# Kernel optimization log

Hardware: AMD Instinct MI355X
Metric: run time of the kernel (lower is better)

Reference implementation:

```python
import jax, jax.numpy as jnp
import numpy as np

IN_CHANNELS = 8
CHANNELS = 8
MASK_OUT_STRIDE = 4


def aligned_bilinear(x, factor):
    # Faithful port of AdelaiDet aligned_bilinear (align_corners=True).
    if factor == 1:
        return x
    n, c, h, w = x.shape
    x = jnp.pad(x, ((0, 0), (0, 0), (0, 1), (0, 1)), mode='edge')
    oh, ow = factor * h + 1, factor * w + 1

    def interp_axis(arr, out_len, axis):
        # align_corners=True from size s+1 -> factor*s+1: src coord = i / factor
        coords = jnp.arange(out_len) / factor
        i0 = jnp.floor(coords).astype(jnp.int32)
        i1 = jnp.minimum(i0 + 1, arr.shape[axis] - 1)
        t = (coords - i0).astype(arr.dtype)
        a0 = jnp.take(arr, i0, axis=axis)
        a1 = jnp.take(arr, i1, axis=axis)
        shp = [1] * arr.ndim
        shp[axis] = out_len
        t = t.reshape(shp)
        return a0 * (1 - t) + a1 * t

    x = interp_axis(x, oh, 2)
    x = interp_axis(x, ow, 3)
    p = factor // 2
    x = jnp.pad(x, ((0, 0), (0, 0), (p, 0), (p, 0)), mode='edge')
    return x[:, :, : oh - 1, : ow - 1]


def setup_inputs() -> dict:
    key = jax.random.key(0)
    ks = jax.random.split(key, 6)
    N, C, H, W = 4, IN_CHANNELS, 112, 200
    n_inst = 200
    stride = 8
    num_gen_params = (C + 2) * CHANNELS + CHANNELS + CHANNELS * CHANNELS + CHANNELS + CHANNELS + 1  # 169
    mask_feats = jax.random.normal(ks[0], (N, C, H, W), dtype=jnp.float32)
    mask_head_params = jax.random.normal(ks[1], (n_inst, num_gen_params), dtype=jnp.float32) * 0.1
    # instance centers anywhere inside the image (in input-image pixel coords)
    instance_locations = jax.random.uniform(ks[2], (n_inst, 2), dtype=jnp.float32) * jnp.array(
        [W * stride, H * stride], dtype=jnp.float32)
    sizes_of_interest = jnp.array([64.0, 128.0, 256.0, 512.0, 1024.0], dtype=jnp.float32)
    im_inds = jax.random.randint(ks[3], (n_inst,), 0, N, dtype=jnp.int32)
    fpn_levels = jax.random.randint(ks[4], (n_inst,), 0, 5, dtype=jnp.int32)
    return {
        'mask_feats': mask_feats,
        'mask_head_params': mask_head_params,
        'instance_locations': instance_locations,
        'sizes_of_interest': sizes_of_interest,
        'im_inds': im_inds,
        'fpn_levels': fpn_levels,
        'mask_feat_stride': stride,
    }


def reference(mask_feats, mask_head_params, instance_locations, sizes_of_interest,
              im_inds, fpn_levels, mask_feat_stride):
    N, C, H, W = mask_feats.shape
    n_inst = mask_head_params.shape[0]
    HW = H * W
    stride = mask_feat_stride  # python int

    # compute_locations: (x, y) pairs, x fastest, at pixel centers (stride//2 offset)
    xs = (jnp.arange(W) * stride + stride // 2).astype(mask_feats.dtype)
    ys = (jnp.arange(H) * stride + stride // 2).astype(mask_feats.dtype)
    gx, gy = jnp.meshgrid(xs, ys, indexing='xy')  # [H, W]
    locations = jnp.stack([gx, gy], axis=-1).reshape(HW, 2)  # [HW, 2]

    # relative coords, normalized by size-of-interest per instance
    rel = instance_locations[:, None, :] - locations[None, :, :]  # [n, HW, 2]
    rel = jnp.transpose(rel, (0, 2, 1))  # [n, 2, HW]
    soi = sizes_of_interest[fpn_levels]  # [n]
    rel = rel / soi[:, None, None]

    feats = mask_feats[im_inds].reshape(n_inst, C, HW)  # [n, C, HW]
    x = jnp.concatenate([rel, feats], axis=1)  # [n, C+2, HW]

    # parse_dynamic_params: split [n, 169] into per-layer 1x1 conv weights/biases
    wn = [(C + 2) * CHANNELS, CHANNELS * CHANNELS, CHANNELS * 1]
    bn = [CHANNELS, CHANNELS, 1]
    sizes = wn + bn
    offs = np.cumsum([0] + sizes)
    parts = [mask_head_params[:, offs[i]:offs[i + 1]] for i in range(len(sizes))]
    w0 = parts[0].reshape(n_inst, CHANNELS, C + 2)
    w1 = parts[1].reshape(n_inst, CHANNELS, CHANNELS)
    w2 = parts[2].reshape(n_inst, 1, CHANNELS)
    b0, b1, b2 = parts[3], parts[4], parts[5]

    # per-instance grouped 1x1 convs == batched matmuls over instances
    x = jax.nn.relu(jnp.einsum('noi,nip->nop', w0, x) + b0[:, :, None])
    x = jax.nn.relu(jnp.einsum('noi,nip->nop', w1, x) + b1[:, :, None])
    x = jnp.einsum('noi,nip->nop', w2, x) + b2[:, :, None]  # [n, 1, HW]

    mask_logits = x.reshape(n_inst, 1, H, W)
    factor = stride // MASK_OUT_STRIDE
    return aligned_bilinear(mask_logits, factor)
```

## Files before the change

### kernel.cpp

```cpp
#include <hip/hip_runtime.h>


#define IN_C   8
#define CHN    8
#define Hh     112
#define Ww     200
#define HWp    (Hh * Ww)
#define OH     224
#define OW     400
#define TY     16
#define RL     9
#define NPIX   (RL * Ww)
#define NPAIR  (NPIX / 2)
#define NTILES (OH / TY)
#define NPARAMS 169

typedef __fp16 f16x2 __attribute__((ext_vector_type(2)));


__global__ __launch_bounds__(256, 4)
void dmh_fused_kernel(const float* __restrict__ feats,
                      const float* __restrict__ params,
                      const float* __restrict__ iloc,
                      const float* __restrict__ soi_tab,
                      const int*   __restrict__ im_inds,
                      const int*   __restrict__ fpn_levels,
                      float* __restrict__ out)
{
    __shared__ uint  h0s[CHN][NPAIR];
    __shared__ float lgt[RL][Ww];

    const int bid  = blockIdx.x;
    const int inst = bid / NTILES;
    const int ty   = bid - inst * NTILES;
    const int y0   = ty * TY;
    const int r_lo = (y0 > 0 ? (y0 - 1) : 0) >> 1;
    const int tid  = threadIdx.x;

    const float* __restrict__ wp = params + inst * NPARAMS;
    const float soi    = soi_tab[fpn_levels[inst]];
    const float inv_s  = 1.0f / soi;
    const float ix     = iloc[inst * 2 + 0];
    const float iy     = iloc[inst * 2 + 1];
    const float* __restrict__ fb = feats + (size_t)im_inds[inst] * (IN_C * HWp);

    {
        float w0r[80];
        #pragma unroll
        for (int i = 0; i < 80; i++) w0r[i] = wp[i];
        #pragma unroll
        for (int i = 0; i < 80; i++) asm volatile("" : "+v"(w0r[i]));

        for (int g = tid; g < NPAIR; g += 256) {
            const int rr = g / (Ww / 2);
            const int c2 = (g - rr * (Ww / 2)) * 2;
            const int r  = r_lo + rr;
            const float* fp = fb + r * Ww + c2;

            float fv0[IN_C], fv1[IN_C];
            #pragma unroll
            for (int ch = 0; ch < IN_C; ch++) {
                const float2 t = *reinterpret_cast<const float2*>(fp + ch * HWp);
                fv0[ch] = t.x; fv1[ch] = t.y;
            }
            const float in1  = (iy - (float)(r * 8 + 4)) * inv_s;
            const float in00 = (ix - (float)(c2 * 8 + 4)) * inv_s;
            const float in01 = (ix - (float)(c2 * 8 + 12)) * inv_s;

            #pragma unroll
            for (int o = 0; o < CHN; o++) {
                const float bo = fmaf(w0r[o * 10 + 1], in1, wp[152 + o]);
                float t0 = fmaf(w0r[o * 10 + 0], in00, bo);
                float t1 = fmaf(w0r[o * 10 + 0], in01, bo);
                #pragma unroll
                for (int i = 0; i < IN_C; i++) {
                    t0 = fmaf(w0r[o * 10 + 2 + i], fv0[i], t0);
                    t1 = fmaf(w0r[o * 10 + 2 + i], fv1[i], t1);
                }
                t0 = fmaxf(t0, 0.0f);
                t1 = fmaxf(t1, 0.0f);
                const f16x2 pk = __builtin_amdgcn_cvt_pkrtz(t0, t1);
                h0s[o][g] = *reinterpret_cast<const uint*>(&pk);
            }
        }
    }
    __syncthreads();

    {
        float w1r[64], w2r[CHN];
        #pragma unroll
        for (int i = 0; i < 64; i++) w1r[i] = wp[80 + i];
        #pragma unroll
        for (int i = 0; i < CHN; i++) w2r[i] = wp[144 + i];
        #pragma unroll
        for (int i = 0; i < 64; i++) asm volatile("" : "+v"(w1r[i]));
        #pragma unroll
        for (int i = 0; i < CHN; i++) asm volatile("" : "+v"(w2r[i]));

        for (int g = tid; g < NPAIR; g += 256) {
            float h00[CHN], h01[CHN];
            #pragma unroll
            for (int i = 0; i < CHN; i++) {
                const uint w = h0s[i][g];
                const f16x2 pk = *reinterpret_cast<const f16x2*>(&w);
                h00[i] = (float)pk.x;
                h01[i] = (float)pk.y;
            }
            float r0 = wp[168], r1 = wp[168];
            #pragma unroll
            for (int o = 0; o < CHN; o++) {
                float a0 = wp[160 + o];
                float a1 = a0;
                #pragma unroll
                for (int i = 0; i < CHN; i++) {
                    a0 = fmaf(w1r[o * 8 + i], h00[i], a0);
                    a1 = fmaf(w1r[o * 8 + i], h01[i], a1);
                }
                a0 = fmaxf(a0, 0.0f);
                a1 = fmaxf(a1, 0.0f);
                r0 = fmaf(w2r[o], a0, r0);
                r1 = fmaf(w2r[o], a1, r1);
            }
            const int rr = g / (Ww / 2);
            const int c2 = (g - rr * (Ww / 2)) * 2;
            *reinterpret_cast<float2*>(&lgt[rr][c2]) = make_float2(r0, r1);
        }
    }
    __syncthreads();

    float* __restrict__ ob = out + (size_t)inst * (OH * OW);
    const int NQ = (TY * OW) / 4;
    for (int q = tid; q < NQ; q += 256) {
        const int dy = q / (OW / 4);
        const int gx = q - dy * (OW / 4);
        const int x  = gx * 4;
        const int y  = y0 + dy;
        const int i  = (y > 0 ? y - 1 : 0);
        const int rr0 = (i >> 1) - r_lo;
        const int r1g = (i >> 1) + (i & 1);
        const int rr1 = (r1g > Hh - 1 ? Hh - 1 : r1g) - r_lo;
        const float wy1 = (i & 1) ? 0.5f : 0.0f;
        const float wy0 = 1.0f - wy1;

        const int cx  = x >> 1;
        const int cm1 = (cx > 0 ? cx - 1 : 0);
        const float a_m = lgt[rr0][cm1], a_0 = lgt[rr0][cx], a_p = lgt[rr0][cx + 1];
        const float b_m = lgt[rr1][cm1], b_0 = lgt[rr1][cx], b_p = lgt[rr1][cx + 1];
        const float Rm = wy0 * a_m + wy1 * b_m;
        const float R0 = wy0 * a_0 + wy1 * b_0;
        const float Rp = wy0 * a_p + wy1 * b_p;

        float4 o4;
        o4.x = 0.5f * (Rm + R0);
        o4.y = R0;
        o4.z = 0.5f * (R0 + Rp);
        o4.w = Rp;
        *reinterpret_cast<float4*>(&ob[y * OW + x]) = o4;
    }
}

extern "C" void kernel_launch(void* const* d_in, const int* in_sizes, int n_in,
                              void* d_out, int out_size, void* d_ws, size_t ws_size,
                              hipStream_t stream) {
    const float* mask_feats = (const float*)d_in[0];
    const float* params     = (const float*)d_in[1];
    const float* iloc       = (const float*)d_in[2];
    const float* soi        = (const float*)d_in[3];
    const int*   im_inds    = (const int*)d_in[4];
    const int*   fpn        = (const int*)d_in[5];
    float* out = (float*)d_out;

    const int n_inst = in_sizes[4];
    dim3 grid(n_inst * NTILES);
    dim3 block(256);
    hipLaunchKernelGGL(dmh_fused_kernel, grid, block, 0, stream,
                       mask_feats, params, iloc, soi, im_inds, fpn, out);
}
```

Measured before the change: 38.59 us.

## Keep per-instance weights in scalar registers and double block size

Per-instance weights, biases and instance scalars are now read through readfirstlane, so the compiler can hold them in SGPRs instead of forcing them into VGPRs with asm barriers. This frees vector registers. The block size rises from 256 to 512 threads with launch bounds asking for 8 blocks per CU, aiming for higher occupancy. The risks are SGPR pressure from roughly 170 scalar values, possible spills, and fewer loop iterations per thread, since each block covers only about 900 pixel pairs.

```diff
diff --git a/kernel.cpp b/kernel.cpp
--- a/kernel.cpp
+++ b/kernel.cpp
@@ -14,11 +14,16 @@
 #define NPAIR  (NPIX / 2)
 #define NTILES (OH / TY)
 #define NPARAMS 169
+#define BLK    512
 
 typedef __fp16 f16x2 __attribute__((ext_vector_type(2)));
 
+__device__ __forceinline__ float rfl(float x) {
+    return __int_as_float(__builtin_amdgcn_readfirstlane(__float_as_int(x)));
+}
 
-__global__ __launch_bounds__(256, 4)
+
+__global__ __launch_bounds__(BLK, 8)
 void dmh_fused_kernel(const float* __restrict__ feats,
                       const float* __restrict__ params,
                       const float* __restrict__ iloc,
@@ -38,20 +43,21 @@
     const int tid  = threadIdx.x;
 
     const float* __restrict__ wp = params + inst * NPARAMS;
-    const float soi    = soi_tab[fpn_levels[inst]];
+    const float soi    = rfl(soi_tab[fpn_levels[inst]]);
     const float inv_s  = 1.0f / soi;
-    const float ix     = iloc[inst * 2 + 0];
-    const float iy     = iloc[inst * 2 + 1];
+    const float ix     = rfl(iloc[inst * 2 + 0]);
+    const float iy     = rfl(iloc[inst * 2 + 1]);
     const float* __restrict__ fb = feats + (size_t)im_inds[inst] * (IN_C * HWp);
 
     {
         float w0r[80];
         #pragma unroll
-        for (int i = 0; i < 80; i++) w0r[i] = wp[i];
+        for (int i = 0; i < 80; i++) w0r[i] = rfl(wp[i]);
+        float b0r[CHN];
         #pragma unroll
-        for (int i = 0; i < 80; i++) asm volatile("" : "+v"(w0r[i]));
+        for (int i = 0; i < CHN; i++) b0r[i] = rfl(wp[152 + i]);
 
-        for (int g = tid; g < NPAIR; g += 256) {
+        for (int g = tid; g < NPAIR; g += BLK) {
             const int rr = g / (Ww / 2);
             const int c2 = (g - rr * (Ww / 2)) * 2;
             const int r  = r_lo + rr;
@@ -69,7 +75,7 @@
 
             #pragma unroll
             for (int o = 0; o < CHN; o++) {
-                const float bo = fmaf(w0r[o * 10 + 1], in1, wp[152 + o]);
+                const float bo = fmaf(w0r[o * 10 + 1], in1, b0r[o]);
                 float t0 = fmaf(w0r[o * 10 + 0], in00, bo);
                 float t1 = fmaf(w0r[o * 10 + 0], in01, bo);
                 #pragma unroll
@@ -87,17 +93,16 @@
     __syncthreads();
 
     {
-        float w1r[64], w2r[CHN];
+        float w1r[64], w2r[CHN], b1r[CHN];
         #pragma unroll
-        for (int i = 0; i < 64; i++) w1r[i] = wp[80 + i];
+        for (int i = 0; i < 64; i++) w1r[i] = rfl(wp[80 + i]);
         #pragma unroll
-        for (int i = 0; i < CHN; i++) w2r[i] = wp[144 + i];
+        for (int i = 0; i < CHN; i++) w2r[i] = rfl(wp[144 + i]);
         #pragma unroll
-        for (int i = 0; i < 64; i++) asm volatile("" : "+v"(w1r[i]));
-        #pragma unroll
-        for (int i = 0; i < CHN; i++) asm volatile("" : "+v"(w2r[i]));
+        for (int i = 0; i < CHN; i++) b1r[i] = rfl(wp[160 + i]);
+        const float b2 = rfl(wp[168]);
 
-        for (int g = tid; g < NPAIR; g += 256) {
+        for (int g = tid; g < NPAIR; g += BLK) {
             float h00[CHN], h01[CHN];
             #pragma unroll
             for (int i = 0; i < CHN; i++) {
@@ -106,10 +111,10 @@
                 h00[i] = (float)pk.x;
                 h01[i] = (float)pk.y;
             }
-            float r0 = wp[168], r1 = wp[168];
+            float r0 = b2, r1 = b2;
             #pragma unroll
             for (int o = 0; o < CHN; o++) {
-                float a0 = wp[160 + o];
+                float a0 = b1r[o];
                 float a1 = a0;
                 #pragma unroll
                 for (int i = 0; i < CHN; i++) {
@@ -130,7 +135,7 @@
 
     float* __restrict__ ob = out + (size_t)inst * (OH * OW);
     const int NQ = (TY * OW) / 4;
-    for (int q = tid; q < NQ; q += 256) {
+    for (int q = tid; q < NQ; q += BLK) {
         const int dy = q / (OW / 4);
         const int gx = q - dy * (OW / 4);
         const int x  = gx * 4;
@@ -172,7 +177,7 @@
 
     const int n_inst = in_sizes[4];
     dim3 grid(n_inst * NTILES);
-    dim3 block(256);
+    dim3 block(BLK);
     hipLaunchKernelGGL(dmh_fused_kernel, grid, block, 0, stream,
                        mask_feats, params, iloc, soi, im_inds, fpn, out);
 }
```

Result: slower. 48.05 us (+24.5%).
